# Kernel tuning notes

Hardware: AMD Instinct MI355X
Metric: run time of the kernel (lower is better)

The kernel has to match this reference:

```python
import jax, jax.numpy as jnp
from jax import lax
import numpy as np

B, L, T, H = 64, 128, 32, 512


def _lstm_cell(x, h, c, Wih, Whh, bih, bhh):
    # torch gate order: i, f, g, o
    g = x @ Wih.T + h @ Whh.T + bih + bhh
    i, f, gg, o = jnp.split(g, 4, axis=-1)
    c = jax.nn.sigmoid(f) * c + jax.nn.sigmoid(i) * jnp.tanh(gg)
    h = jax.nn.sigmoid(o) * jnp.tanh(c)
    return h, c


def setup_inputs() -> dict:
    key = jax.random.key(0)
    ks = jax.random.split(key, 16)
    s = 0.03
    seq = jax.random.normal(ks[0], (B, L), jnp.float32)
    seq_m = jax.random.randint(ks[1], (B, 1), 1, L + 1)  # lengths in [1, L]
    # zero-pad beyond length so the nonzero-mask in forward is meaningful
    seq = jnp.where(jnp.arange(L)[None, :] < seq_m, seq, 0.0)
    target = jax.random.normal(ks[2], (B, T), jnp.float32)
    p = {
        'Wih_e': jax.random.normal(ks[3], (4 * H, 1), jnp.float32) * s,
        'Whh_e': jax.random.normal(ks[4], (4 * H, H), jnp.float32) * s,
        'bih_e': jax.random.normal(ks[5], (4 * H,), jnp.float32) * s,
        'bhh_e': jax.random.normal(ks[6], (4 * H,), jnp.float32) * s,
        'Wih_d': jax.random.normal(ks[7], (4 * H, 1), jnp.float32) * s,
        'Whh_d': jax.random.normal(ks[8], (4 * H, H), jnp.float32) * s,
        'bih_d': jax.random.normal(ks[9], (4 * H,), jnp.float32) * s,
        'bhh_d': jax.random.normal(ks[10], (4 * H,), jnp.float32) * s,
        'We': jax.random.normal(ks[11], (H, H), jnp.float32) * s,
        'be': jax.random.normal(ks[12], (H,), jnp.float32) * s,
        'Wd': jax.random.normal(ks[13], (H, H), jnp.float32) * s,
        'bd': jax.random.normal(ks[14], (H,), jnp.float32) * s,
        'v': jnp.ones((H,), jnp.float32),  # Parameter(torch.ones(H))
    }
    return dict(seq=seq, seq_m=seq_m, target=target, **p)


def reference(seq, seq_m, target, Wih_e, Whh_e, bih_e, bhh_e,
              Wih_d, Whh_d, bih_d, bhh_d, We, be, Wd, bd, v):
    Bn, Ln = seq.shape
    Tn = target.shape[1]
    Hn = Whh_e.shape[1]

    # ---- encoder: step-by-step LSTM over seq (feat dim = 1) ----
    def enc_step(carry, x_t):
        h, c = carry
        h, c = _lstm_cell(x_t, h, c, Wih_e, Whh_e, bih_e, bhh_e)
        return (h, c), (h, c)

    x_seq = seq.T[:, :, None]  # [L, B, 1]
    h0 = jnp.zeros((Bn, Hn), seq.dtype)
    _, (h_all, c_all) = lax.scan(enc_step, (h0, h0), x_seq)  # [L, B, H]
    e = jnp.transpose(h_all, (1, 0, 2))  # [B, L, H]

    # per-example encoder state at time seq_m-1 (layer 0)
    lens = seq_m[:, 0] - 1
    bidx = jnp.arange(Bn)
    h_init = h_all[lens, bidx]  # [B, H]
    c_init = c_all[lens, bidx]

    # in-place sq[:,0,:] = 0.1 from the source; mask = nonzero entries
    seq_mod = seq.at[:, 0].set(0.1)
    mask = seq_mod != 0.0  # [B, L]

    # ---- decoder with pointer attention; e_linear re-applied to e each step ----
    def dec_step(carry, i):
        h, c, d_in, e_cur = carry
        x = jnp.where(i == 0, target[:, 0:1],
                      jnp.where(i == 1, target[:, 1:2], d_in))  # [B, 1]
        h, c = _lstm_cell(x, h, c, Wih_d, Whh_d, bih_d, bhh_d)
        e_cur = e_cur @ We.T + be              # cumulative e_linear (faithful)
        d = h @ Wd.T + bd                      # [B, H]
        scores = jnp.einsum('blh,h->bl', jnp.tanh(e_cur + d[:, None, :]), v)
        logits = jnp.where(mask, scores, scores - 1000.0)
        p = jax.nn.softmax(logits, axis=-1)    # [B, L]
        ptr = jnp.argmax(p, axis=-1)           # [B]
        d_next = jnp.take_along_axis(seq_mod, ptr[:, None], axis=1)  # [B, 1]
        return (h, c, d_next, e_cur), p

    init = (h_init, c_init, target[:, 0:1], e)
    _, ps = lax.scan(dec_step, init, jnp.arange(Tn))  # [T, B, L]
    return jnp.transpose(ps, (1, 0, 2))  # [B, T, L]
```

## Files before the change

kernel.cpp:

```cpp
#include <hip/hip_runtime.h>
#include <cstddef>
#include <cstdint>

#define BN 64
#define LN 128
#define TN 32
#define HN 512
#define GN 2048

typedef __attribute__((ext_vector_type(8))) short short8;
typedef __attribute__((ext_vector_type(4))) float f32x4;

__device__ __forceinline__ float fsig(float x)  { return 1.0f / (1.0f + __expf(-x)); }
__device__ __forceinline__ float ftanh(float x) { return 1.0f - 2.0f / (__expf(2.0f * x) + 1.0f); }

__device__ __forceinline__ unsigned short bf16r(float v) {
  unsigned int u = __float_as_uint(v);
  u += 0x7FFFu + ((u >> 16) & 1u);
  return (unsigned short)(u >> 16);
}
__device__ __forceinline__ float bf2f(unsigned short h) {
  return __uint_as_float((unsigned int)h << 16);
}
__device__ __forceinline__ void sysstore(float* p, float v) {
  __hip_atomic_store(p, v, __ATOMIC_RELAXED, __HIP_MEMORY_SCOPE_SYSTEM);
}
__device__ __forceinline__ unsigned sysloadU(const unsigned* p) {
  return __hip_atomic_load(p, __ATOMIC_RELAXED, __HIP_MEMORY_SCOPE_SYSTEM);
}
__device__ __forceinline__ void sysstoreU(unsigned* p, unsigned v) {
  __hip_atomic_store(p, v, __ATOMIC_RELAXED, __HIP_MEMORY_SCOPE_SYSTEM);
}

__global__ __launch_bounds__(256) void k_tpack(
    const float* __restrict__ Whh_e, const float* __restrict__ Whh_d,
    float* __restrict__ Wt4E, float* __restrict__ Wt4D) {
  int blk = blockIdx.x;
  const float* src = (blk >> 7) ? Whh_d : Whh_e;
  float* dst = (blk >> 7) ? Wt4D : Wt4E;
  int r = blk & 127;
  int kt = r >> 4, ct = r & 15;
  int t = threadIdx.x;
  __shared__ float L[4][32][65];
  int cl = t >> 3, k8 = (t & 7) * 8;
#pragma unroll
  for (int g = 0; g < 4; ++g) {
    float4 a = *(const float4*)&src[(size_t)(g * 512 + ct * 32 + cl) * 512 + kt * 64 + k8];
    float4 b = *(const float4*)&src[(size_t)(g * 512 + ct * 32 + cl) * 512 + kt * 64 + k8 + 4];
    L[g][cl][k8 + 0] = a.x; L[g][cl][k8 + 1] = a.y; L[g][cl][k8 + 2] = a.z; L[g][cl][k8 + 3] = a.w;
    L[g][cl][k8 + 4] = b.x; L[g][cl][k8 + 5] = b.y; L[g][cl][k8 + 6] = b.z; L[g][cl][k8 + 7] = b.w;
  }
  __syncthreads();
  int kl = t >> 2, c8 = (t & 3) * 8;
#pragma unroll
  for (int i = 0; i < 8; ++i) {
    int c = c8 + i;
    float4 v = make_float4(L[0][c][kl], L[1][c][kl], L[2][c][kl], L[3][c][kl]);
    *(float4*)&dst[((size_t)(kt * 64 + kl) * 512 + ct * 32 + c) * 4] = v;
  }
}

__global__ __launch_bounds__(256) void k_tr(
    const float* __restrict__ We, const float* __restrict__ Wd,
    float* __restrict__ M0, float* __restrict__ WdT) {
  int blk = blockIdx.x;
  const float* src = (blk >> 8) ? Wd : We;
  float* dst = (blk >> 8) ? WdT : M0;
  int r = blk & 255;
  int rt = r >> 4, ct = r & 15;
  int t = threadIdx.x;
  __shared__ float T[32][33];
  int jl = t >> 3, m4 = (t & 7) * 4;
  float4 a = *(const float4*)&src[(size_t)(ct * 32 + jl) * 512 + rt * 32 + m4];
  T[jl][m4 + 0] = a.x; T[jl][m4 + 1] = a.y; T[jl][m4 + 2] = a.z; T[jl][m4 + 3] = a.w;
  __syncthreads();
  int ml = t >> 3, j4 = (t & 7) * 4;
  float4 v = make_float4(T[j4 + 0][ml], T[j4 + 1][ml], T[j4 + 2][ml], T[j4 + 3][ml]);
  *(float4*)&dst[(size_t)(rt * 32 + ml) * 512 + ct * 32 + j4] = v;
}

__global__ __launch_bounds__(256) void k_small(
    const float* __restrict__ Wih_e, const float* __restrict__ Wih_d,
    const float* __restrict__ bih_e, const float* __restrict__ bhh_e,
    const float* __restrict__ bih_d, const float* __restrict__ bhh_d,
    const float* __restrict__ be,
    float* __restrict__ WihE4, float* __restrict__ WihD4,
    float* __restrict__ bsE4, float* __restrict__ bsD4,
    float* __restrict__ zvec, unsigned int* __restrict__ cnt,
    unsigned int* __restrict__ flags, float* __restrict__ cva0) {
  int idx = blockIdx.x * 256 + threadIdx.x;
  if (idx < 2048) { int c = idx >> 2, g = idx & 3; WihE4[idx] = Wih_e[g * 512 + c]; }
  else if (idx < 4096) { int r = idx - 2048; int c = r >> 2, g = r & 3; WihD4[r] = Wih_d[g * 512 + c]; }
  else if (idx < 6144) { int r = idx - 4096; int c = r >> 2, g = r & 3; bsE4[r] = bih_e[g * 512 + c] + bhh_e[g * 512 + c]; }
  else if (idx < 8192) { int r = idx - 6144; int c = r >> 2, g = r & 3; bsD4[r] = bih_d[g * 512 + c] + bhh_d[g * 512 + c]; }
  else if (idx < 8704) { zvec[idx - 8192] = 0.f; }
  else if (idx < 8736) { cnt[idx - 8704] = 0u; }
  else if (idx < 9248) { flags[idx - 8736] = 0u; }
  else if (idx < 9760) { cva0[idx - 9248] = be[idx - 9248]; }
}

__global__ __launch_bounds__(512) void k_enc(
    const float* __restrict__ seq, const int* __restrict__ seq_m,
    const float* __restrict__ WihE4, const float* __restrict__ Wt4E,
    const float* __restrict__ bsE4,
    float* __restrict__ e, float* __restrict__ hdec, float* __restrict__ cdec,
    float* __restrict__ hx , unsigned int* __restrict__ eflags) {
  int blk = blockIdx.x;
  int g = ((blk & 7) << 1) | ((blk >> 3) & 1);
  int s = blk >> 4;
  int b0 = g * 4;
  int t = threadIdx.x;
  int c_idx = t & 31, kq = t >> 5;
  int c = s * 32 + c_idx;
  __shared__ float hs[4][HN];
  __shared__ float P[16][4][32][4];
  for (int i = t; i < 4 * HN; i += 512) ((float*)hs)[i] = 0.f;
  int ebb = t >> 5, eci = t & 31;
  float cstate = 0.f;
  float4 wih = make_float4(0, 0, 0, 0), bs4 = make_float4(0, 0, 0, 0);
  int len = -2;
  if (t < 128) {
    int ec = s * 32 + eci;
    wih = *(const float4*)&WihE4[ec * 4];
    bs4 = *(const float4*)&bsE4[ec * 4];
    len = seq_m[b0 + ebb] - 1;
  }
  const float* wbase = Wt4E + ((size_t)(kq * 32) * 512 + c) * 4;
  __syncthreads();
  for (int st = 0; st < LN; ++st) {
    if (st > 0) {
      const float4* src4 = (const float4*)(hx + (size_t)(st - 1) * (BN * HN) + (size_t)b0 * HN);
      ((float4*)hs)[t] = src4[t];
      __syncthreads();
    }
    float4 acc0 = make_float4(0, 0, 0, 0), acc1 = acc0, acc2 = acc0, acc3 = acc0;
#pragma unroll
    for (int kk4 = 0; kk4 < 8; ++kk4) {
      float4 h0 = *(const float4*)&hs[0][kq * 32 + kk4 * 4];
      float4 h1 = *(const float4*)&hs[1][kq * 32 + kk4 * 4];
      float4 h2 = *(const float4*)&hs[2][kq * 32 + kk4 * 4];
      float4 h3 = *(const float4*)&hs[3][kq * 32 + kk4 * 4];
      const float* wp = wbase + (size_t)(kk4 * 4) * 2048;
#pragma unroll
      for (int u = 0; u < 4; ++u) {
        float4 w = *(const float4*)(wp + (size_t)u * 2048);
        float hu0 = (&h0.x)[u], hu1 = (&h1.x)[u], hu2 = (&h2.x)[u], hu3 = (&h3.x)[u];
        acc0.x += w.x * hu0; acc0.y += w.y * hu0; acc0.z += w.z * hu0; acc0.w += w.w * hu0;
        acc1.x += w.x * hu1; acc1.y += w.y * hu1; acc1.z += w.z * hu1; acc1.w += w.w * hu1;
        acc2.x += w.x * hu2; acc2.y += w.y * hu2; acc2.z += w.z * hu2; acc2.w += w.w * hu2;
        acc3.x += w.x * hu3; acc3.y += w.y * hu3; acc3.z += w.z * hu3; acc3.w += w.w * hu3;
      }
    }
    *(float4*)&P[kq][0][c_idx][0] = acc0;
    *(float4*)&P[kq][1][c_idx][0] = acc1;
    *(float4*)&P[kq][2][c_idx][0] = acc2;
    *(float4*)&P[kq][3][c_idx][0] = acc3;
    __syncthreads();
    if (t < 128) {
      int b = b0 + ebb, ec = s * 32 + eci;
      float4 gsum = make_float4(0, 0, 0, 0);
#pragma unroll
      for (int q = 0; q < 16; ++q) {
        float4 p = *(const float4*)&P[q][ebb][eci][0];
        gsum.x += p.x; gsum.y += p.y; gsum.z += p.z; gsum.w += p.w;
      }
      float x = seq[b * LN + st];
      float gi = gsum.x + x * wih.x + bs4.x;
      float gf = gsum.y + x * wih.y + bs4.y;
      float gg = gsum.z + x * wih.z + bs4.z;
      float go = gsum.w + x * wih.w + bs4.w;
      float cn = fsig(gf) * cstate + fsig(gi) * ftanh(gg);
      cstate = cn;
      float hn = fsig(go) * ftanh(cn);
      e[((size_t)b * LN + st) * HN + ec] = hn;
      sysstore(&hx[(size_t)st * (BN * HN) + (size_t)b * HN + ec], hn);
      if (st == len) { hdec[(size_t)b * HN + ec] = hn; cdec[(size_t)b * HN + ec] = cn; }
    }
    __syncthreads();
    if (t == 0) sysstoreU(&eflags[g * 16 + s], (unsigned)(st + 1));
    if (t < 16) {
      unsigned v;
      do {
        v = sysloadU(&eflags[g * 16 + t]);
        if (v < (unsigned)(st + 1)) __builtin_amdgcn_s_sleep(2);
      } while (v < (unsigned)(st + 1));
    }
    __syncthreads();
  }
}

__global__ __launch_bounds__(256) void k_gemm(
    const float* __restrict__ Ab, const float* __restrict__ Bb,
    const float* __restrict__ Cvb, float* __restrict__ Ob,
    size_t Asz, size_t Bsz, size_t Cvsz, size_t Osz) {
  int z = blockIdx.z;
  const float* A = Ab + (size_t)z * Asz;
  const float* B = Bb + (size_t)z * Bsz;
  const float* CV = Cvb + (size_t)z * Cvsz;
  float* O = Ob + (size_t)z * Osz;
  int tn = blockIdx.x * 128;
  int tm = blockIdx.y * 128;
  int t = threadIdx.x;
  __shared__ float As[8][132];
  __shared__ float Bs[8][132];
  int ar = t >> 1, ak4 = (t & 1) * 4;
  int bk2 = t >> 5, bj = (t & 31) * 4;
  int ty = t >> 4, tx = t & 15;
  float acc[8][8];
#pragma unroll
  for (int i = 0; i < 8; ++i)
#pragma unroll
    for (int j = 0; j < 8; ++j) acc[i][j] = 0.f;
  for (int k0 = 0; k0 < 512; k0 += 8) {
    float4 av = *(const float4*)&A[(size_t)(tm + ar) * 512 + k0 + ak4];
    float4 bv = *(const float4*)&B[(size_t)(k0 + bk2) * 512 + tn + bj];
    __syncthreads();
    As[ak4 + 0][ar] = av.x; As[ak4 + 1][ar] = av.y; As[ak4 + 2][ar] = av.z; As[ak4 + 3][ar] = av.w;
    *(float4*)&Bs[bk2][bj] = bv;
    __syncthreads();
#pragma unroll
    for (int kk = 0; kk < 8; ++kk) {
      float4 A0 = *(const float4*)&As[kk][ty * 8];
      float4 A1 = *(const float4*)&As[kk][ty * 8 + 4];
      float4 B0 = *(const float4*)&Bs[kk][tx * 8];
      float4 B1 = *(const float4*)&Bs[kk][tx * 8 + 4];
      float am[8] = {A0.x, A0.y, A0.z, A0.w, A1.x, A1.y, A1.z, A1.w};
      float bn[8] = {B0.x, B0.y, B0.z, B0.w, B1.x, B1.y, B1.z, B1.w};
#pragma unroll
      for (int i2 = 0; i2 < 8; ++i2)
#pragma unroll
        for (int j2 = 0; j2 < 8; ++j2) acc[i2][j2] += am[i2] * bn[j2];
    }
  }
  float4 cv0 = *(const float4*)&CV[tn + tx * 8];
  float4 cv1 = *(const float4*)&CV[tn + tx * 8 + 4];
  float cvv[8] = {cv0.x, cv0.y, cv0.z, cv0.w, cv1.x, cv1.y, cv1.z, cv1.w};
#pragma unroll
  for (int r = 0; r < 8; ++r) {
    float4 o0, o1;
    o0.x = acc[r][0] + cvv[0]; o0.y = acc[r][1] + cvv[1]; o0.z = acc[r][2] + cvv[2]; o0.w = acc[r][3] + cvv[3];
    o1.x = acc[r][4] + cvv[4]; o1.y = acc[r][5] + cvv[5]; o1.z = acc[r][6] + cvv[6]; o1.w = acc[r][7] + cvv[7];
    *(float4*)&O[(size_t)(tm + ty * 8 + r) * 512 + tn + tx * 8]     = o0;
    *(float4*)&O[(size_t)(tm + ty * 8 + r) * 512 + tn + tx * 8 + 4] = o1;
  }
}

__global__ __launch_bounds__(256) void k_cvec(
    const float* __restrict__ be, const float* __restrict__ Mall, float* __restrict__ vtmp) {
  int k = blockIdx.x, t = threadIdx.x;
  const float* M = Mall + (size_t)k * 262144;
  float a0 = 0.f, a1 = 0.f;
  for (int m = 0; m < 512; ++m) {
    float bm = be[m];
    a0 += bm * M[(size_t)m * 512 + t];
    a1 += bm * M[(size_t)m * 512 + t + 256];
  }
  vtmp[(size_t)k * 512 + t] = a0;
  vtmp[(size_t)k * 512 + t + 256] = a1;
}

__global__ __launch_bounds__(512) void k_cpref(
    const float* __restrict__ be, const float* __restrict__ vtmp, float* __restrict__ cva) {
  int j = threadIdx.x;
  float run = be[j];
  for (int i = 0; i < 32; ++i) {
    cva[(size_t)i * 512 + j] = run;
    if (i < 31) run += vtmp[(size_t)i * 512 + j];
  }
}

__global__ __launch_bounds__(256) void k_packM(
    const float* __restrict__ Mall, unsigned short* __restrict__ MhiT,
    unsigned short* __restrict__ MloT) {
  int i = blockIdx.y;
  int tile = blockIdx.x;
  int kt = tile >> 4, nt = tile & 15;
  int t = threadIdx.x;
  __shared__ unsigned short Lh[32][36];
  __shared__ unsigned short Ll[32][36];
  int kl = t >> 3, n4 = (t & 7) * 4;
  float4 v = *(const float4*)&Mall[(size_t)i * 262144 + (size_t)(kt * 32 + kl) * 512 + nt * 32 + n4];
#pragma unroll
  for (int u = 0; u < 4; ++u) {
    float f = (&v.x)[u];
    unsigned short h = bf16r(f);
    Lh[kl][n4 + u] = h;
    Ll[kl][n4 + u] = bf16r(f - bf2f(h));
  }
  __syncthreads();
  int nl = t >> 3, k4 = (t & 7) * 4;
  size_t dst = (size_t)i * 262144 + (size_t)(nt * 32 + nl) * 512 + kt * 32 + k4;
  *(ushort4*)&MhiT[dst] = make_ushort4(Lh[k4][nl], Lh[k4 + 1][nl], Lh[k4 + 2][nl], Lh[k4 + 3][nl]);
  *(ushort4*)&MloT[dst] = make_ushort4(Ll[k4][nl], Ll[k4 + 1][nl], Ll[k4 + 2][nl], Ll[k4 + 3][nl]);
}

__global__ __launch_bounds__(512, 1) void k_dec2(
    const float* __restrict__ target, const float* __restrict__ seq,
    const float* __restrict__ Wt4D, const float* __restrict__ WihD4,
    const float* __restrict__ bsD4,
    const float* __restrict__ WdT, const float* __restrict__ bd,
    const float* __restrict__ vv, const float* __restrict__ e,
    const unsigned short* __restrict__ MhiT, const unsigned short* __restrict__ MloT,
    const float* __restrict__ cva,
    const float* __restrict__ hdec0, const float* __restrict__ cdec0,
    float* __restrict__ hgN,
    float* __restrict__ dvecN,
    float* __restrict__ scoresN,
    unsigned int* __restrict__ dflags,
    float* __restrict__ out) {
  int blk = blockIdx.x;
  int bq = blk >> 4, s = blk & 15;
  int b0 = bq * 4;
  int pb = blk >> 2, plt = blk & 3;
  int t = threadIdx.x;
  int lane = t & 63, w = t >> 6;
  int m16 = lane & 15, quad = lane >> 4;

  __shared__ unsigned short Ah[32][520];
  __shared__ unsigned short Al[32][520];
  __shared__ float hs[4][HN];
  __shared__ float P[16][4][32][4];
  __shared__ float Q[16][4][32];
  __shared__ float sc[4][LN];
  __shared__ float xs[4];
  __shared__ float Dv[HN];
  __shared__ float pw[8][32];

  {
    const float4* esrc = (const float4*)(e + ((size_t)pb * 128 + plt * 32) * HN);
    for (int idx = t; idx < 4096; idx += 512) {
      float4 v = esrc[idx];
      int r = idx >> 7, c4 = (idx & 127) * 4;
#pragma unroll
      for (int u = 0; u < 4; ++u) {
        float f = (&v.x)[u];
        unsigned short h = bf16r(f);
        Ah[r][c4 + u] = h;
        Al[r][c4 + u] = bf16r(f - bf2f(h));
      }
    }
  }
  float creg = 0.f;
  if (t < 128) creg = cdec0[(size_t)(b0 + (t >> 5)) * HN + s * 32 + (t & 31)];
  unsigned int bphase = 0;
  __syncthreads();

  auto gbar = [&]() {
    ++bphase;
    __syncthreads();
    if (t == 0) sysstoreU(&dflags[blk], bphase);
    unsigned v;
    do {
      v = sysloadU(&dflags[t & 255]);
      if (v < bphase) __builtin_amdgcn_s_sleep(2);
    } while (v < bphase);
    __syncthreads();
  };

  for (int i = 0; i < TN; ++i) {
    if (i > 0) {
      const float* ssrc = scoresN + (size_t)(i - 1) * 8192 + (size_t)b0 * 128;
      sc[t >> 7][t & 127] = ssrc[t];
    }
    __syncthreads();
    if (w < 4) {
      int b = b0 + w;
      if (i == 0) {
        if (lane == 0) xs[w] = target[b * TN + 0];
      } else {
        float v0 = sc[w][lane], v1 = sc[w][64 + lane];
        bool m0 = (lane == 0) || (seq[b * LN + lane] != 0.f);
        bool m1 = (seq[b * LN + 64 + lane] != 0.f);
        v0 = m0 ? v0 : v0 - 1000.f;
        v1 = m1 ? v1 : v1 - 1000.f;
        float mx; int ix;
        if (v0 >= v1) { mx = v0; ix = lane; } else { mx = v1; ix = 64 + lane; }
#pragma unroll
        for (int off = 32; off >= 1; off >>= 1) {
          float ov = __shfl_down(mx, off);
          int   oi = __shfl_down(ix, off);
          if (ov > mx || (ov == mx && oi < ix)) { mx = ov; ix = oi; }
        }
        mx = __shfl(mx, 0); ix = __shfl(ix, 0);
        float e0 = __expf(v0 - mx), e1 = __expf(v1 - mx);
        float sum = e0 + e1;
#pragma unroll
        for (int off = 32; off >= 1; off >>= 1) sum += __shfl_down(sum, off);
        sum = __shfl(sum, 0);
        float inv = 1.0f / sum;
        if (s == 0) {
          out[((size_t)b * TN + i - 1) * LN + lane] = e0 * inv;
          out[((size_t)b * TN + i - 1) * LN + 64 + lane] = e1 * inv;
        }
        if (lane == 0)
          xs[w] = (i == 1) ? target[b * TN + 1]
                           : ((ix == 0) ? 0.1f : seq[b * LN + ix]);
      }
    }
    {
      const float* hb = (i == 0) ? (hdec0 + (size_t)b0 * HN)
                                 : (hgN + (size_t)(i - 1) * (BN * HN) + (size_t)b0 * HN);
      ((float4*)hs)[t] = ((const float4*)hb)[t];
    }
    __syncthreads();
    {
      int j_idx = t & 31, kq = t >> 5;
      int j = s * 32 + j_idx;
      const float* wbase = Wt4D + ((size_t)(kq * 32) * 512 + j) * 4;
      float4 acc0 = make_float4(0, 0, 0, 0), acc1 = acc0, acc2 = acc0, acc3 = acc0;
#pragma unroll
      for (int kk4 = 0; kk4 < 8; ++kk4) {
        float4 h0 = *(const float4*)&hs[0][kq * 32 + kk4 * 4];
        float4 h1 = *(const float4*)&hs[1][kq * 32 + kk4 * 4];
        float4 h2 = *(const float4*)&hs[2][kq * 32 + kk4 * 4];
        float4 h3 = *(const float4*)&hs[3][kq * 32 + kk4 * 4];
        const float* wp = wbase + (size_t)(kk4 * 4) * 2048;
#pragma unroll
        for (int u = 0; u < 4; ++u) {
          float4 wv = *(const float4*)(wp + (size_t)u * 2048);
          float hu0 = (&h0.x)[u], hu1 = (&h1.x)[u], hu2 = (&h2.x)[u], hu3 = (&h3.x)[u];
          acc0.x += wv.x * hu0; acc0.y += wv.y * hu0; acc0.z += wv.z * hu0; acc0.w += wv.w * hu0;
          acc1.x += wv.x * hu1; acc1.y += wv.y * hu1; acc1.z += wv.z * hu1; acc1.w += wv.w * hu1;
          acc2.x += wv.x * hu2; acc2.y += wv.y * hu2; acc2.z += wv.z * hu2; acc2.w += wv.w * hu2;
          acc3.x += wv.x * hu3; acc3.y += wv.y * hu3; acc3.z += wv.z * hu3; acc3.w += wv.w * hu3;
        }
      }
      *(float4*)&P[kq][0][j_idx][0] = acc0;
      *(float4*)&P[kq][1][j_idx][0] = acc1;
      *(float4*)&P[kq][2][j_idx][0] = acc2;
      *(float4*)&P[kq][3][j_idx][0] = acc3;
    }
    __syncthreads();
    if (t < 128) {
      int bb = t >> 5, ji = t & 31;
      int b = b0 + bb, jj = s * 32 + ji;
      float4 gsum = make_float4(0, 0, 0, 0);
#pragma unroll
      for (int q = 0; q < 16; ++q) {
        float4 p = *(const float4*)&P[q][bb][ji][0];
        gsum.x += p.x; gsum.y += p.y; gsum.z += p.z; gsum.w += p.w;
      }
      float x = xs[bb];
      float4 wih = *(const float4*)&WihD4[jj * 4];
      float4 b4 = *(const float4*)&bsD4[jj * 4];
      float gi = gsum.x + x * wih.x + b4.x;
      float gf = gsum.y + x * wih.y + b4.y;
      float gg = gsum.z + x * wih.z + b4.z;
      float go = gsum.w + x * wih.w + b4.w;
      float cn = fsig(gf) * creg + fsig(gi) * ftanh(gg);
      creg = cn;
      float hn = fsig(go) * ftanh(cn);
      sysstore(&hgN[(size_t)i * (BN * HN) + (size_t)b * HN + jj], hn);
    }
    gbar();

    {
      const float* hb = hgN + (size_t)i * (BN * HN) + (size_t)b0 * HN;
      ((float4*)hs)[t] = ((const float4*)hb)[t];
    }
    __syncthreads();
    {
      int j_idx = t & 31, kq = t >> 5;
      int j = s * 32 + j_idx;
      float a0 = 0, a1 = 0, a2 = 0, a3 = 0;
#pragma unroll
      for (int kk4 = 0; kk4 < 8; ++kk4) {
        float4 h0 = *(const float4*)&hs[0][kq * 32 + kk4 * 4];
        float4 h1 = *(const float4*)&hs[1][kq * 32 + kk4 * 4];
        float4 h2 = *(const float4*)&hs[2][kq * 32 + kk4 * 4];
        float4 h3 = *(const float4*)&hs[3][kq * 32 + kk4 * 4];
#pragma unroll
        for (int u = 0; u < 4; ++u) {
          float wv = WdT[(size_t)(kq * 32 + kk4 * 4 + u) * 512 + j];
          a0 += wv * (&h0.x)[u]; a1 += wv * (&h1.x)[u];
          a2 += wv * (&h2.x)[u]; a3 += wv * (&h3.x)[u];
        }
      }
      Q[kq][0][j_idx] = a0; Q[kq][1][j_idx] = a1;
      Q[kq][2][j_idx] = a2; Q[kq][3][j_idx] = a3;
    }
    __syncthreads();
    if (t < 128) {
      int bb = t >> 5, ji = t & 31;
      int jj = s * 32 + ji;
      float d = bd[jj] + cva[(size_t)i * HN + jj];
#pragma unroll
      for (int q = 0; q < 16; ++q) d += Q[q][bb][ji];
      sysstore(&dvecN[(size_t)i * (BN * HN) + (size_t)(b0 + bb) * HN + jj], d);
    }
    gbar();

    Dv[t] = dvecN[(size_t)i * (BN * HN) + (size_t)pb * HN + t];
    __syncthreads();
    {
      f32x4 acc[2][4];
#pragma unroll
      for (int mf = 0; mf < 2; ++mf)
#pragma unroll
        for (int nt = 0; nt < 4; ++nt) acc[mf][nt] = (f32x4){0.f, 0.f, 0.f, 0.f};
      const size_t ibase = (size_t)i * 262144;
      for (int kc = 0; kc < 16; ++kc) {
        int ka = kc * 32 + quad * 8;
        short8 ah0 = *(const short8*)&Ah[m16][ka];
        short8 ah1 = *(const short8*)&Ah[16 + m16][ka];
        short8 al0 = *(const short8*)&Al[m16][ka];
        short8 al1 = *(const short8*)&Al[16 + m16][ka];
#pragma unroll
        for (int nt = 0; nt < 4; ++nt) {
          int n = w * 64 + nt * 16 + m16;
          size_t baddr = ibase + (size_t)n * 512 + ka;
          short8 bh = *(const short8*)&MhiT[baddr];
          short8 bl = *(const short8*)&MloT[baddr];
          acc[0][nt] = __builtin_amdgcn_mfma_f32_16x16x32_bf16(ah0, bh, acc[0][nt], 0, 0, 0);
          acc[0][nt] = __builtin_amdgcn_mfma_f32_16x16x32_bf16(ah0, bl, acc[0][nt], 0, 0, 0);
          acc[0][nt] = __builtin_amdgcn_mfma_f32_16x16x32_bf16(al0, bh, acc[0][nt], 0, 0, 0);
          acc[1][nt] = __builtin_amdgcn_mfma_f32_16x16x32_bf16(ah1, bh, acc[1][nt], 0, 0, 0);
          acc[1][nt] = __builtin_amdgcn_mfma_f32_16x16x32_bf16(ah1, bl, acc[1][nt], 0, 0, 0);
          acc[1][nt] = __builtin_amdgcn_mfma_f32_16x16x32_bf16(al1, bh, acc[1][nt], 0, 0, 0);
        }
      }
      float dloc[4], vloc[4];
#pragma unroll
      for (int nt = 0; nt < 4; ++nt) {
        int cidx = w * 64 + nt * 16 + m16;
        dloc[nt] = Dv[cidx];
        vloc[nt] = vv[cidx];
      }
#pragma unroll
      for (int mf = 0; mf < 2; ++mf)
#pragma unroll
        for (int r = 0; r < 4; ++r) {
          float sv = 0.f;
#pragma unroll
          for (int nt = 0; nt < 4; ++nt)
            sv += vloc[nt] * ftanh(acc[mf][nt][r] + dloc[nt]);
          sv += __shfl_xor(sv, 1);
          sv += __shfl_xor(sv, 2);
          sv += __shfl_xor(sv, 4);
          sv += __shfl_xor(sv, 8);
          if (m16 == 0) pw[w][mf * 16 + quad * 4 + r] = sv;
        }
    }
    __syncthreads();
    if (t < 32) {
      float ssum = 0.f;
#pragma unroll
      for (int w2 = 0; w2 < 8; ++w2) ssum += pw[w2][t];
      sysstore(&scoresN[(size_t)i * 8192 + (size_t)pb * 128 + plt * 32 + t], ssum);
    }
    gbar();
  }

  {
    const float* ssrc = scoresN + (size_t)31 * 8192 + (size_t)b0 * 128;
    sc[t >> 7][t & 127] = ssrc[t];
  }
  __syncthreads();
  if (s == 0 && w < 4) {
    int b = b0 + w;
    float v0 = sc[w][lane], v1 = sc[w][64 + lane];
    bool m0 = (lane == 0) || (seq[b * LN + lane] != 0.f);
    bool m1 = (seq[b * LN + 64 + lane] != 0.f);
    v0 = m0 ? v0 : v0 - 1000.f;
    v1 = m1 ? v1 : v1 - 1000.f;
    float mx = fmaxf(v0, v1);
#pragma unroll
    for (int off = 32; off >= 1; off >>= 1) mx = fmaxf(mx, __shfl_down(mx, off));
    mx = __shfl(mx, 0);
    float e0 = __expf(v0 - mx), e1 = __expf(v1 - mx);
    float sum = e0 + e1;
#pragma unroll
    for (int off = 32; off >= 1; off >>= 1) sum += __shfl_down(sum, off);
    sum = __shfl(sum, 0);
    float inv = 1.0f / sum;
    out[((size_t)b * TN + 31) * LN + lane] = e0 * inv;
    out[((size_t)b * TN + 31) * LN + 64 + lane] = e1 * inv;
  }
}

__global__ __launch_bounds__(256) void k_score(
    const float* __restrict__ E, const float* __restrict__ M,
    const float* __restrict__ cv, const float* __restrict__ dvec,
    const float* __restrict__ vvx, float* __restrict__ scores) {
  int b = blockIdx.x >> 3, lt = blockIdx.x & 7;
  int l0 = lt * 16;
  int t = threadIdx.x;
  int ty = t >> 6, tx = t & 63;
  __shared__ float As[16][20];
  __shared__ float Bs[16][516];
  float acc[4][8];
#pragma unroll
  for (int r = 0; r < 4; ++r)
#pragma unroll
    for (int u = 0; u < 8; ++u) acc[r][u] = 0.f;
  int all = t >> 4, akk = t & 15;
  int bkr = t >> 4, bc = (t & 15) * 32;
  for (int k0 = 0; k0 < 512; k0 += 16) {
    __syncthreads();
    As[all][akk] = E[((size_t)b * LN + l0 + all) * 512 + k0 + akk];
#pragma unroll
    for (int u = 0; u < 8; ++u)
      *(float4*)&Bs[bkr][bc + u * 4] = *(const float4*)&M[(size_t)(k0 + bkr) * 512 + bc + u * 4];
    __syncthreads();
#pragma unroll
    for (int kk = 0; kk < 16; ++kk) {
      float a0 = As[ty * 4 + 0][kk];
      float a1 = As[ty * 4 + 1][kk];
      float a2 = As[ty * 4 + 2][kk];
      float a3 = As[ty * 4 + 3][kk];
      float4 bA = *(const float4*)&Bs[kk][tx * 8];
      float4 bB = *(const float4*)&Bs[kk][tx * 8 + 4];
      float bn[8] = {bA.x, bA.y, bA.z, bA.w, bB.x, bB.y, bB.z, bB.w};
#pragma unroll
      for (int u = 0; u < 8; ++u) {
        acc[0][u] += a0 * bn[u];
        acc[1][u] += a1 * bn[u];
        acc[2][u] += a2 * bn[u];
        acc[3][u] += a3 * bn[u];
      }
    }
  }
  float4 cv0 = *(const float4*)&cv[tx * 8];
  float4 cv1 = *(const float4*)&cv[tx * 8 + 4];
  float4 dv0 = *(const float4*)&dvec[(size_t)b * HN + tx * 8];
  float4 dv1 = *(const float4*)&dvec[(size_t)b * HN + tx * 8 + 4];
  float4 vA = *(const float4*)&vvx[tx * 8];
  float4 vB = *(const float4*)&vvx[tx * 8 + 4];
  float cvv[8] = {cv0.x + dv0.x, cv0.y + dv0.y, cv0.z + dv0.z, cv0.w + dv0.w,
                  cv1.x + dv1.x, cv1.y + dv1.y, cv1.z + dv1.z, cv1.w + dv1.w};
  float vr[8] = {vA.x, vA.y, vA.z, vA.w, vB.x, vB.y, vB.z, vB.w};
#pragma unroll
  for (int r = 0; r < 4; ++r) {
    float sacc = 0.f;
#pragma unroll
    for (int u = 0; u < 8; ++u) sacc += vr[u] * ftanh(acc[r][u] + cvv[u]);
#pragma unroll
    for (int off = 32; off >= 1; off >>= 1) sacc += __shfl_down(sacc, off);
    if (tx == 0) scores[(size_t)b * LN + l0 + ty * 4 + r] = sacc;
  }
}

__global__ __launch_bounds__(256) void k_dstep(
    int stepi,
    const float* __restrict__ target, const float* __restrict__ seq,
    const float* __restrict__ scores,
    const float* __restrict__ Wt4D, const float* __restrict__ WihD4,
    const float* __restrict__ bsD4,
    const float* __restrict__ hread, float* __restrict__ hwrite,
    float* __restrict__ cdec, float* __restrict__ out) {
  int blk = blockIdx.x;
  int bq = blk >> 4, s = blk & 15;
  int b0 = bq * 4;
  int t = threadIdx.x;
  int lane = t & 63, w = t >> 6;
  __shared__ float xs[4];
  __shared__ float hs[4][HN];
  __shared__ float P[8][4][32][4];
  {
    int b = b0 + w;
    if (stepi == 0) {
      if (lane == 0) xs[w] = target[b * TN + 0];
    } else {
      float v0 = scores[b * LN + lane];
      float v1 = scores[b * LN + 64 + lane];
      bool m0 = (lane == 0) || (seq[b * LN + lane] != 0.f);
      bool m1 = (seq[b * LN + 64 + lane] != 0.f);
      v0 = m0 ? v0 : v0 - 1000.f;
      v1 = m1 ? v1 : v1 - 1000.f;
      float mx; int ix;
      if (v0 >= v1) { mx = v0; ix = lane; } else { mx = v1; ix = 64 + lane; }
#pragma unroll
      for (int off = 32; off >= 1; off >>= 1) {
        float ov = __shfl_down(mx, off);
        int   oi = __shfl_down(ix, off);
        if (ov > mx || (ov == mx && oi < ix)) { mx = ov; ix = oi; }
      }
      mx = __shfl(mx, 0); ix = __shfl(ix, 0);
      float e0 = __expf(v0 - mx), e1 = __expf(v1 - mx);
      float sum = e0 + e1;
#pragma unroll
      for (int off = 32; off >= 1; off >>= 1) sum += __shfl_down(sum, off);
      sum = __shfl(sum, 0);
      float inv = 1.0f / sum;
      if (s == 0) {
        out[((size_t)b * TN + stepi - 1) * LN + lane] = e0 * inv;
        out[((size_t)b * TN + stepi - 1) * LN + 64 + lane] = e1 * inv;
      }
      if (lane == 0)
        xs[w] = (stepi == 1) ? target[b * TN + 1]
                             : ((ix == 0) ? 0.1f : seq[b * LN + ix]);
    }
  }
  for (int i = t; i < 4 * HN; i += 256)
    hs[i >> 9][i & 511] = hread[(size_t)(b0 + (i >> 9)) * HN + (i & 511)];
  __syncthreads();
  int j_idx = t & 31, kq = t >> 5;
  int j = s * 32 + j_idx;
  const float* wbase = Wt4D + ((size_t)(kq * 64) * 512 + j) * 4;
  float4 acc0 = make_float4(0, 0, 0, 0), acc1 = acc0, acc2 = acc0, acc3 = acc0;
#pragma unroll 4
  for (int kk4 = 0; kk4 < 16; ++kk4) {
    float4 h0 = *(const float4*)&hs[0][kq * 64 + kk4 * 4];
    float4 h1 = *(const float4*)&hs[1][kq * 64 + kk4 * 4];
    float4 h2 = *(const float4*)&hs[2][kq * 64 + kk4 * 4];
    float4 h3 = *(const float4*)&hs[3][kq * 64 + kk4 * 4];
    const float* wp = wbase + (size_t)(kk4 * 4) * 2048;
#pragma unroll
    for (int u = 0; u < 4; ++u) {
      float4 wv = *(const float4*)(wp + (size_t)u * 2048);
      float hu0 = (&h0.x)[u], hu1 = (&h1.x)[u], hu2 = (&h2.x)[u], hu3 = (&h3.x)[u];
      acc0.x += wv.x * hu0; acc0.y += wv.y * hu0; acc0.z += wv.z * hu0; acc0.w += wv.w * hu0;
      acc1.x += wv.x * hu1; acc1.y += wv.y * hu1; acc1.z += wv.z * hu1; acc1.w += wv.w * hu1;
      acc2.x += wv.x * hu2; acc2.y += wv.y * hu2; acc2.z += wv.z * hu2; acc2.w += wv.w * hu2;
      acc3.x += wv.x * hu3; acc3.y += wv.y * hu3; acc3.z += wv.z * hu3; acc3.w += wv.w * hu3;
    }
  }
  *(float4*)&P[kq][0][j_idx][0] = acc0;
  *(float4*)&P[kq][1][j_idx][0] = acc1;
  *(float4*)&P[kq][2][j_idx][0] = acc2;
  *(float4*)&P[kq][3][j_idx][0] = acc3;
  __syncthreads();
  if (t < 128) {
    int bb = t >> 5, ji = t & 31;
    int b = b0 + bb, jj = s * 32 + ji;
    float4 gsum = make_float4(0, 0, 0, 0);
#pragma unroll
    for (int q = 0; q < 8; ++q) {
      float4 p = *(const float4*)&P[q][bb][ji][0];
      gsum.x += p.x; gsum.y += p.y; gsum.z += p.z; gsum.w += p.w;
    }
    float x = xs[bb];
    float4 wih = *(const float4*)&WihD4[jj * 4];
    float4 b4 = *(const float4*)&bsD4[jj * 4];
    float gi = gsum.x + x * wih.x + b4.x;
    float gf = gsum.y + x * wih.y + b4.y;
    float gg = gsum.z + x * wih.z + b4.z;
    float go = gsum.w + x * wih.w + b4.w;
    float cold = cdec[(size_t)b * HN + jj];
    float cn = fsig(gf) * cold + fsig(gi) * ftanh(gg);
    float hn = fsig(go) * ftanh(cn);
    cdec[(size_t)b * HN + jj] = cn;
    hwrite[(size_t)b * HN + jj] = hn;
  }
}

__global__ __launch_bounds__(256) void k_dproj(
    const float* __restrict__ hnew, const float* __restrict__ WdT,
    const float* __restrict__ bd, float* __restrict__ dvec) {
  int blk = blockIdx.x;
  int bq = blk >> 4, s = blk & 15;
  int b0 = bq * 4;
  int t = threadIdx.x;
  int j_idx = t & 31, kq = t >> 5;
  int j = s * 32 + j_idx;
  __shared__ float hs[4][HN];
  __shared__ float Q[8][4][32];
  for (int i = t; i < 4 * HN; i += 256)
    hs[i >> 9][i & 511] = hnew[(size_t)(b0 + (i >> 9)) * HN + (i & 511)];
  __syncthreads();
  float a0 = 0, a1 = 0, a2 = 0, a3 = 0;
#pragma unroll 4
  for (int kk4 = 0; kk4 < 16; ++kk4) {
    float4 h0 = *(const float4*)&hs[0][kq * 64 + kk4 * 4];
    float4 h1 = *(const float4*)&hs[1][kq * 64 + kk4 * 4];
    float4 h2 = *(const float4*)&hs[2][kq * 64 + kk4 * 4];
    float4 h3 = *(const float4*)&hs[3][kq * 64 + kk4 * 4];
#pragma unroll
    for (int u = 0; u < 4; ++u) {
      float wv = WdT[(size_t)(kq * 64 + kk4 * 4 + u) * 512 + j];
      a0 += wv * (&h0.x)[u]; a1 += wv * (&h1.x)[u];
      a2 += wv * (&h2.x)[u]; a3 += wv * (&h3.x)[u];
    }
  }
  Q[kq][0][j_idx] = a0; Q[kq][1][j_idx] = a1; Q[kq][2][j_idx] = a2; Q[kq][3][j_idx] = a3;
  __syncthreads();
  if (t < 128) {
    int bb = t >> 5, ji = t & 31;
    int jj = s * 32 + ji;
    float d = bd[jj];
#pragma unroll
    for (int q = 0; q < 8; ++q) d += Q[q][bb][ji];
    dvec[(size_t)(b0 + bb) * HN + jj] = d;
  }
}

__global__ __launch_bounds__(64) void k_fin(
    const float* __restrict__ scores, const float* __restrict__ seq,
    float* __restrict__ out) {
  int b = blockIdx.x, lane = threadIdx.x;
  float v0 = scores[b * LN + lane];
  float v1 = scores[b * LN + 64 + lane];
  bool m0 = (lane == 0) || (seq[b * LN + lane] != 0.f);
  bool m1 = (seq[b * LN + 64 + lane] != 0.f);
  v0 = m0 ? v0 : v0 - 1000.f;
  v1 = m1 ? v1 : v1 - 1000.f;
  float mx = fmaxf(v0, v1);
#pragma unroll
  for (int off = 32; off >= 1; off >>= 1) mx = fmaxf(mx, __shfl_down(mx, off));
  mx = __shfl(mx, 0);
  float e0 = __expf(v0 - mx), e1 = __expf(v1 - mx);
  float sum = e0 + e1;
#pragma unroll
  for (int off = 32; off >= 1; off >>= 1) sum += __shfl_down(sum, off);
  sum = __shfl(sum, 0);
  float inv = 1.0f / sum;
  out[((size_t)b * TN + 31) * LN + lane] = e0 * inv;
  out[((size_t)b * TN + 31) * LN + 64 + lane] = e1 * inv;
}

extern "C" void kernel_launch(void* const* d_in, const int* in_sizes, int n_in,
                              void* d_out, int out_size, void* d_ws, size_t ws_size,
                              hipStream_t stream) {
  const float* seq    = (const float*)d_in[0];
  const int*   seq_m  = (const int*)  d_in[1];
  const float* target = (const float*)d_in[2];
  const float* Wih_e  = (const float*)d_in[3];
  const float* Whh_e  = (const float*)d_in[4];
  const float* bih_e  = (const float*)d_in[5];
  const float* bhh_e  = (const float*)d_in[6];
  const float* Wih_d  = (const float*)d_in[7];
  const float* Whh_d  = (const float*)d_in[8];
  const float* bih_d  = (const float*)d_in[9];
  const float* bhh_d  = (const float*)d_in[10];
  const float* We     = (const float*)d_in[11];
  const float* be     = (const float*)d_in[12];
  const float* Wd     = (const float*)d_in[13];
  const float* bd     = (const float*)d_in[14];
  const float* vv     = (const float*)d_in[15];
  float* out = (float*)d_out;
  float* W = (float*)d_ws;

  size_t o = 0;
  float* Wt4E = W + o; o += 1048576;
  float* Wt4D = W + o; o += 1048576;
  float* WdT  = W + o; o += 262144;
  float* WihE4 = W + o; o += 2048;
  float* WihD4 = W + o; o += 2048;
  float* bsE4 = W + o; o += 2048;
  float* bsD4 = W + o; o += 2048;
  float* zvec = W + o; o += 512;
  unsigned int* cnt = (unsigned int*)(W + o); o += 32;
  unsigned int* flags = (unsigned int*)(W + o); o += 512;
  float* cva  = W + o; o += 16384;
  float* vtmp = W + o; o += 15872;
  float* hdec = W + o; o += 32768;
  float* cdec = W + o; o += 32768;
  float* dvecL = W + o; o += 32768;
  float* scoresL = W + o; o += 8192;
  float* hleg = W + o; o += 65536;
  float* e    = W + o; o += 4194304;
  size_t fixed = o;
  float* Mall = W + fixed;
  float* hgN     = Mall;
  float* dvecN   = Mall + 1048576;
  float* scoresN = Mall + 2097152;
  unsigned short* MhiT = (unsigned short*)(W + fixed + 8388608);
  unsigned short* MloT = MhiT + 8388608;
  float* hx = (float*)MhiT;

  size_t t1need = (fixed + 8388608ull + 4194304ull + 4194304ull) * 4;
  int tier = (ws_size >= t1need) ? 1 : 2;

  unsigned int* eflags = flags;
  unsigned int* dflags = flags + 256;

  k_tpack<<<256, 256, 0, stream>>>(Whh_e, Whh_d, Wt4E, Wt4D);
  k_tr<<<512, 256, 0, stream>>>(We, Wd, Mall, WdT);
  k_small<<<39, 256, 0, stream>>>(Wih_e, Wih_d, bih_e, bhh_e, bih_d, bhh_d, be,
                                  WihE4, WihD4, bsE4, bsD4, zvec, cnt, flags, cva);
  if (tier == 1) {
    k_enc<<<256, 512, 0, stream>>>(seq, seq_m, WihE4, Wt4E, bsE4, e, hdec, cdec,
                                   hx, eflags);
    for (int r = 0; r < 5; ++r) {
      int p = 1 << r;
      dim3 gp(4, 4, p);
      k_gemm<<<gp, 256, 0, stream>>>(Mall, Mall + (size_t)(p - 1) * 262144, zvec,
                                     Mall + (size_t)p * 262144, 262144, 0, 0, 262144);
    }
    k_cvec<<<31, 256, 0, stream>>>(be, Mall, vtmp);
    k_cpref<<<1, 512, 0, stream>>>(be, vtmp, cva);
    k_packM<<<dim3(256, 32), 256, 0, stream>>>(Mall, MhiT, MloT);
    k_dec2<<<256, 512, 0, stream>>>(target, seq, Wt4D, WihD4, bsD4, WdT, bd, vv, e,
                                    MhiT, MloT, cva, hdec, cdec,
                                    hgN, dvecN, scoresN, dflags, out);
  } else {
    float* hx2 = Mall;
    k_enc<<<256, 512, 0, stream>>>(seq, seq_m, WihE4, Wt4E, bsE4, e, hdec, cdec,
                                   hx2, eflags);
    k_tr<<<512, 256, 0, stream>>>(We, Wd, Mall, WdT);
    for (int i = 0; i < TN; ++i) {
      const float* Mi; const float* ci;
      if (i == 0) { Mi = Mall; ci = cva; }
      else {
        float* Msrc = (i == 1) ? Mall : Mall + (size_t)(1 + (i & 1)) * 262144;
        float* Mdst = Mall + (size_t)(1 + ((i - 1) & 1)) * 262144;
        dim3 gp(4, 4, 1);
        k_gemm<<<gp, 256, 0, stream>>>(Msrc, Mall, zvec, Mdst, 0, 0, 0, 0);
        k_cpref<<<1, 512, 0, stream>>>(be, vtmp, cva);
        Mi = Mdst; ci = cva;
      }
      float* hw = hleg + (size_t)(i & 1) * 32768;
      const float* hrd = (i == 0) ? hdec : hleg + (size_t)((i - 1) & 1) * 32768;
      k_dstep<<<256, 256, 0, stream>>>(i, target, seq, scoresL, Wt4D, WihD4, bsD4,
                                       hrd, hw, cdec, out);
      k_dproj<<<256, 256, 0, stream>>>(hw, WdT, bd, dvecL);
      k_score<<<512, 256, 0, stream>>>(e, Mi, ci, dvecL, vv, scoresL);
    }
    k_fin<<<64, 64, 0, stream>>>(scoresL, seq, out);
  }
}
```

Before: 2.829 ms.

## Fuse decoder Wd projection into LSTM step and use centralized grid barrier

Each block now computes a partial Wd·h product from its own freshly computed 32 hidden units and writes per-slice partials to a double-buffered buffer. Consumers then sum the 16 slices directly, which removes one full grid barrier per decoder step and the separate h reload/GEMV phase. The grid barrier also changes from all-to-all flag polling (every block reads 256 flags) to a master block that gathers the arrivals and publishes a generation counter. This adds an extra hop through block 0 and more partial-sum traffic in global memory.

```diff
diff --git a/kernel.cpp b/kernel.cpp
--- a/kernel.cpp
+++ b/kernel.cpp
@@ -21,6 +21,9 @@
 }
 __device__ __forceinline__ float bf2f(unsigned short h) {
   return __uint_as_float((unsigned int)h << 16);
+}
+__device__ __forceinline__ float sysload(const float* p) {
+  return __hip_atomic_load(p, __ATOMIC_RELAXED, __HIP_MEMORY_SCOPE_SYSTEM);
 }
 __device__ __forceinline__ void sysstore(float* p, float v) {
   __hip_atomic_store(p, v, __ATOMIC_RELAXED, __HIP_MEMORY_SCOPE_SYSTEM);
@@ -95,8 +98,8 @@
   else if (idx < 8192) { int r = idx - 6144; int c = r >> 2, g = r & 3; bsD4[r] = bih_d[g * 512 + c] + bhh_d[g * 512 + c]; }
   else if (idx < 8704) { zvec[idx - 8192] = 0.f; }
   else if (idx < 8736) { cnt[idx - 8704] = 0u; }
-  else if (idx < 9248) { flags[idx - 8736] = 0u; }
-  else if (idx < 9760) { cva0[idx - 9248] = be[idx - 9248]; }
+  else if (idx < 9376) { flags[idx - 8736] = 0u; }
+  else if (idx < 9888) { cva0[idx - 9376] = be[idx - 9376]; }
 }
 
 __global__ __launch_bounds__(512) void k_enc(
@@ -304,9 +307,9 @@
     const float* __restrict__ cva,
     const float* __restrict__ hdec0, const float* __restrict__ cdec0,
     float* __restrict__ hgN,
-    float* __restrict__ dvecN,
+    float* __restrict__ pd2,
     float* __restrict__ scoresN,
-    unsigned int* __restrict__ dflags,
+    unsigned int* __restrict__ dflags, unsigned int* __restrict__ dgen,
     float* __restrict__ out) {
   int blk = blockIdx.x;
   int bq = blk >> 4, s = blk & 15;
@@ -320,7 +323,7 @@
   __shared__ unsigned short Al[32][520];
   __shared__ float hs[4][HN];
   __shared__ float P[16][4][32][4];
-  __shared__ float Q[16][4][32];
+  __shared__ float hnew_s[4][32];
   __shared__ float sc[4][LN];
   __shared__ float xs[4];
   __shared__ float Dv[HN];
@@ -349,11 +352,16 @@
     ++bphase;
     __syncthreads();
     if (t == 0) sysstoreU(&dflags[blk], bphase);
-    unsigned v;
-    do {
-      v = sysloadU(&dflags[t & 255]);
-      if (v < bphase) __builtin_amdgcn_s_sleep(2);
-    } while (v < bphase);
+    if (blk == 0) {
+      if (t < 256) {
+        while (sysloadU(&dflags[t]) < bphase) __builtin_amdgcn_s_sleep(2);
+      }
+      __syncthreads();
+      if (t == 0) sysstoreU(dgen, bphase);
+    }
+    if (t == 0) {
+      while (sysloadU(dgen) < bphase) __builtin_amdgcn_s_sleep(2);
+    }
     __syncthreads();
   };
 
@@ -450,47 +458,37 @@
       float cn = fsig(gf) * creg + fsig(gi) * ftanh(gg);
       creg = cn;
       float hn = fsig(go) * ftanh(cn);
+      hnew_s[bb][ji] = hn;
       sysstore(&hgN[(size_t)i * (BN * HN) + (size_t)b * HN + jj], hn);
     }
+    __syncthreads();
+    {
+      float pdv0 = 0.f, pdv1 = 0.f, pdv2 = 0.f, pdv3 = 0.f;
+      const float* wdbase = WdT + (size_t)(s * 32) * 512 + t;
+#pragma unroll 8
+      for (int k = 0; k < 32; ++k) {
+        float wv = wdbase[(size_t)k * 512];
+        pdv0 += wv * hnew_s[0][k];
+        pdv1 += wv * hnew_s[1][k];
+        pdv2 += wv * hnew_s[2][k];
+        pdv3 += wv * hnew_s[3][k];
+      }
+      float* pdst = pd2 + ((size_t)(i & 1) * 16 + s) * (BN * HN / 16) + (size_t)b0 * 512 + t;
+      sysstore(pdst,               pdv0);
+      sysstore(pdst + 512,         pdv1);
+      sysstore(pdst + 1024,        pdv2);
+      sysstore(pdst + 1536,        pdv3);
+    }
     gbar();
 
     {
-      const float* hb = hgN + (size_t)i * (BN * HN) + (size_t)b0 * HN;
-      ((float4*)hs)[t] = ((const float4*)hb)[t];
-    }
-    __syncthreads();
-    {
-      int j_idx = t & 31, kq = t >> 5;
-      int j = s * 32 + j_idx;
-      float a0 = 0, a1 = 0, a2 = 0, a3 = 0;
-#pragma unroll
-      for (int kk4 = 0; kk4 < 8; ++kk4) {
-        float4 h0 = *(const float4*)&hs[0][kq * 32 + kk4 * 4];
-        float4 h1 = *(const float4*)&hs[1][kq * 32 + kk4 * 4];
-        float4 h2 = *(const float4*)&hs[2][kq * 32 + kk4 * 4];
-        float4 h3 = *(const float4*)&hs[3][kq * 32 + kk4 * 4];
-#pragma unroll
-        for (int u = 0; u < 4; ++u) {
-          float wv = WdT[(size_t)(kq * 32 + kk4 * 4 + u) * 512 + j];
-          a0 += wv * (&h0.x)[u]; a1 += wv * (&h1.x)[u];
-          a2 += wv * (&h2.x)[u]; a3 += wv * (&h3.x)[u];
-        }
-      }
-      Q[kq][0][j_idx] = a0; Q[kq][1][j_idx] = a1;
-      Q[kq][2][j_idx] = a2; Q[kq][3][j_idx] = a3;
-    }
-    __syncthreads();
-    if (t < 128) {
-      int bb = t >> 5, ji = t & 31;
-      int jj = s * 32 + ji;
-      float d = bd[jj] + cva[(size_t)i * HN + jj];
-#pragma unroll
-      for (int q = 0; q < 16; ++q) d += Q[q][bb][ji];
-      sysstore(&dvecN[(size_t)i * (BN * HN) + (size_t)(b0 + bb) * HN + jj], d);
-    }
-    gbar();
-
-    Dv[t] = dvecN[(size_t)i * (BN * HN) + (size_t)pb * HN + t];
+      float dv = bd[t] + cva[(size_t)i * HN + t];
+      const float* psrc = pd2 + (size_t)(i & 1) * 16 * (BN * HN / 16) + (size_t)pb * 512 + t;
+#pragma unroll
+      for (int s2 = 0; s2 < 16; ++s2)
+        dv += sysload(psrc + (size_t)s2 * (BN * HN / 16));
+      Dv[t] = dv;
+    }
     __syncthreads();
     {
       f32x4 acc[2][4];
@@ -840,7 +838,7 @@
   float* bsD4 = W + o; o += 2048;
   float* zvec = W + o; o += 512;
   unsigned int* cnt = (unsigned int*)(W + o); o += 32;
-  unsigned int* flags = (unsigned int*)(W + o); o += 512;
+  unsigned int* flags = (unsigned int*)(W + o); o += 640;
   float* cva  = W + o; o += 16384;
   float* vtmp = W + o; o += 15872;
   float* hdec = W + o; o += 32768;
@@ -852,8 +850,8 @@
   size_t fixed = o;
   float* Mall = W + fixed;
   float* hgN     = Mall;
-  float* dvecN   = Mall + 1048576;
-  float* scoresN = Mall + 2097152;
+  float* scoresN = Mall + 1048576;
+  float* pd2     = Mall + 1048576 + 262144;
   unsigned short* MhiT = (unsigned short*)(W + fixed + 8388608);
   unsigned short* MloT = MhiT + 8388608;
   float* hx = (float*)MhiT;
@@ -863,6 +861,7 @@
 
   unsigned int* eflags = flags;
   unsigned int* dflags = flags + 256;
+  unsigned int* dgen   = flags + 512;
 
   k_tpack<<<256, 256, 0, stream>>>(Whh_e, Whh_d, Wt4E, Wt4D);
   k_tr<<<512, 256, 0, stream>>>(We, Wd, Mall, WdT);
@@ -882,7 +881,7 @@
     k_packM<<<dim3(256, 32), 256, 0, stream>>>(Mall, MhiT, MloT);
     k_dec2<<<256, 512, 0, stream>>>(target, seq, Wt4D, WihD4, bsD4, WdT, bd, vv, e,
                                     MhiT, MloT, cva, hdec, cdec,
-                                    hgN, dvecN, scoresN, dflags, out);
+                                    hgN, pd2, scoresN, dflags, dgen, out);
   } else {
     float* hx2 = Mall;
     k_enc<<<256, 512, 0, stream>>>(seq, seq_m, WihE4, Wt4E, bsE4, e, hdec, cdec,
```

Result: faster. 2.411 ms (-14.8%).
